# Kernel tuning notes

Hardware: AMD Instinct MI355X
Metric: run time of the kernel (lower is better)

Reference implementation:

```python
import jax, jax.numpy as jnp
import numpy as np
import math

NH, NR, HD, QK, ITERS = 8, 8, 64, 32, 4


def _pe(seq_len, dim):
    n = 1.0 / (1.0 + math.exp(-1))
    pos = np.arange(seq_len, dtype=np.float64)[:, None]
    i = np.arange(0, dim, 2, dtype=np.float64)[None, :]
    pe = np.zeros((seq_len, dim), np.float32)
    pe[:, 0::2] = n * np.sin(pos / 10000 ** (2 * i / dim))
    pe[:, 1::2] = n * np.cos(pos / 10000 ** (2 * (i + 1) / dim))
    return jnp.asarray(pe)


def _ln(x, g, b, eps=1e-5):
    m = x.mean(-1, keepdims=True)
    v = ((x - m) ** 2).mean(-1, keepdims=True)
    return (x - m) * jax.lax.rsqrt(v + eps) * g + b


def _comp_attn(x, norm1_g, norm1_b, norm2_g, norm2_b, q_w, q_b, k_w, k_b,
               v_w, v_b, qv_w, qv_b, score_w, score_b, final_w, final_b,
               ffn1_w, ffn1_b, ffn2_w, ffn2_b):
    B, S, D = x.shape
    res = x
    h = _ln(x, norm1_g, norm1_b)
    q = (h @ q_w + q_b).reshape(B, S, NH, HD).transpose(0, 2, 1, 3) / math.sqrt(HD)  # [B,nh,S,hd]
    k = (h @ k_w + k_b).reshape(B, S, NH, HD)                                         # [B,S,nh,hd]
    v = (h @ v_w + v_b).reshape(B, S, NR, HD)                                         # [B,S,nr,hd]
    score = jax.nn.softmax(jnp.einsum('bhqd,bkhd->bhqk', q, k), axis=-1)              # [B,nh,S,S]
    out = jnp.einsum('bhqk,bkrd->bqhrd', score, v)                                    # [B,S,nh,nr,hd]
    qv = (h @ qv_w + qv_b).reshape(B, S, NH, QK)
    qv_e = jnp.broadcast_to(qv[:, :, :, None, :], (B, S, NH, NR, QK))
    in_ = jnp.concatenate([qv_e, out], axis=-1)                                       # [B,S,nh,nr,qk+hd]
    comp = jax.nn.softmax(in_ @ score_w + score_b, axis=3)                            # [B,S,nh,nr,1]
    o = (comp * out).sum(axis=3).reshape(B, S, D)
    o = o @ final_w + final_b
    x = res + o
    res2 = x
    h2 = _ln(x, norm2_g, norm2_b)
    ff = jax.nn.relu(h2 @ ffn1_w + ffn1_b) @ ffn2_w + ffn2_b  # dropout identity (eval)
    return res2 + ff


def reference(img, qst, conv_w, conv_b, qrep_w, qrep_b, cls_token, map_w, map_b,
              norm1_g, norm1_b, norm2_g, norm2_b, q_w, q_b, k_w, k_b, v_w, v_b,
              qv_w, qv_b, score_w, score_b, final_w, final_b,
              ffn1_w, ffn1_b, ffn2_w, ffn2_b, out_w, out_b):
    B = img.shape[0]
    H = conv_w.shape[0]  # 256
    pe = _pe(25, H)
    # patch embedding: conv 15x15 stride 15 -> [B,H,5,5]
    p = jax.lax.conv_general_dilated(img, conv_w, (15, 15), 'VALID',
                                     dimension_numbers=('NCHW', 'OIHW', 'NCHW'))
    p = p + conv_b[None, :, None, None]
    p = p.reshape(B, H, 25).transpose(0, 2, 1) + pe[None]       # [B,25,H]
    cls = jnp.broadcast_to(cls_token, (B, 1, H))
    emb = jnp.concatenate([cls, p], axis=1)                      # [B,26,H]
    que = (qst @ qrep_w + qrep_b)[:, None, :]
    que = jnp.broadcast_to(que, (B, 26, H))
    x = jnp.concatenate([emb, que], axis=-1)                     # [B,26,2H]
    x = x @ map_w + map_b                                        # [B,26,D]
    for _ in range(ITERS):
        x = _comp_attn(x, norm1_g, norm1_b, norm2_g, norm2_b, q_w, q_b, k_w, k_b,
                       v_w, v_b, qv_w, qv_b, score_w, score_b, final_w, final_b,
                       ffn1_w, ffn1_b, ffn2_w, ffn2_b)
    y = x[:, 0, :] @ out_w + out_b
    return jax.nn.log_softmax(y, axis=1)


def setup_inputs() -> dict:
    key = jax.random.key(0)
    ks = iter(jax.random.split(key, 64))
    def rn(shape, s=0.02):
        return jax.random.normal(next(ks), shape, jnp.float32) * s
    B, D, H = 256, 512, 256
    return {
        'img': jax.random.normal(next(ks), (B, 3, 75, 75), jnp.float32),
        'qst': jax.random.normal(next(ks), (B, 18), jnp.float32),
        'conv_w': rn((H, 3, 15, 15)), 'conv_b': rn((H,)),
        'qrep_w': rn((18, H)), 'qrep_b': rn((H,)),
        'cls_token': rn((1, 1, H), 1.0),
        'map_w': rn((2 * H, D)), 'map_b': rn((D,)),
        'norm1_g': jnp.ones((D,), jnp.float32), 'norm1_b': jnp.zeros((D,), jnp.float32),
        'norm2_g': jnp.ones((D,), jnp.float32), 'norm2_b': jnp.zeros((D,), jnp.float32),
        'q_w': rn((D, D)), 'q_b': rn((D,)),
        'k_w': rn((D, D)), 'k_b': rn((D,)),
        'v_w': rn((D, NR * HD)), 'v_b': rn((NR * HD,)),
        'qv_w': rn((D, QK * NH)), 'qv_b': rn((QK * NH,)),
        'score_w': rn((HD + QK, 1)), 'score_b': rn((1,)),
        'final_w': rn((D, D)), 'final_b': rn((D,)),
        'ffn1_w': rn((D, 2 * D)), 'ffn1_b': rn((2 * D,)),
        'ffn2_w': rn((2 * D, D)), 'ffn2_b': rn((D,)),
        'out_w': rn((D, 10)), 'out_b': rn((10,)),
    }
```

## Files before the change

kernel.cpp:

```cpp
#include <hip/hip_runtime.h>
#include <math.h>

#define NB 256
#define SEQ 26
#define TOK (NB*SEQ)
#define DIM 512

typedef unsigned short u16;
typedef __attribute__((ext_vector_type(8))) short short8_t;
typedef __attribute__((ext_vector_type(4))) float floatx4;

__device__ inline u16 f2bf(float f) {
    union { float f; unsigned u; } v; v.f = f;
    unsigned r = v.u + 0x7fffu + ((v.u >> 16) & 1u);
    return (u16)(r >> 16);
}
__device__ inline float bf2f(u16 u) {
    union { unsigned u; float f; } v; v.u = ((unsigned)u) << 16; return v.f;
}

__device__ __forceinline__ void gload_lds16(const u16* g, u16* l) {
    __builtin_amdgcn_global_load_lds((const __attribute__((address_space(1))) void*)g,
                                     (__attribute__((address_space(3))) void*)l, 16, 0, 0);
}

__global__ void prep_all(const float* __restrict__ q_w, const float* __restrict__ k_w,
                         const float* __restrict__ v_w, const float* __restrict__ final_w,
                         const float* __restrict__ ffn1_w, const float* __restrict__ ffn2_w,
                         const float* __restrict__ map_w, const float* __restrict__ conv_w,
                         const float* __restrict__ q_b, const float* __restrict__ k_b,
                         const float* __restrict__ v_b,
                         u16* __restrict__ qkvT, u16* __restrict__ finT,
                         u16* __restrict__ f1T, u16* __restrict__ f2T,
                         u16* __restrict__ mapT, u16* __restrict__ cwT,
                         float* __restrict__ qkvb) {
    __shared__ float lds[64][65];
    int blk = blockIdx.x;
    int t = threadIdx.x;
    if (blk < 544) {
        const float* W; u16* Wt; int K, N, tbase;
        if (blk < 64)       { W = q_w;     Wt = qkvT;            K = 512;  N = 512;  tbase = 0;   }
        else if (blk < 128) { W = k_w;     Wt = qkvT + 512*512;  K = 512;  N = 512;  tbase = 64;  }
        else if (blk < 192) { W = v_w;     Wt = qkvT + 1024*512; K = 512;  N = 512;  tbase = 128; }
        else if (blk < 256) { W = final_w; Wt = finT;            K = 512;  N = 512;  tbase = 192; }
        else if (blk < 384) { W = ffn1_w;  Wt = f1T;             K = 512;  N = 1024; tbase = 256; }
        else if (blk < 512) { W = ffn2_w;  Wt = f2T;             K = 1024; N = 512;  tbase = 384; }
        else                { W = map_w;   Wt = mapT;            K = 256;  N = 512;  tbase = 512; }
        int tloc = blk - tbase;
        int ntn = N >> 6;
        int n0 = (tloc % ntn) * 64, k0 = (tloc / ntn) * 64;
        int j = t & 63, i0 = t >> 6;
        #pragma unroll
        for (int p = 0; p < 16; ++p) {
            int i = i0*16 + p;
            lds[i][j] = W[(size_t)(k0+i)*N + n0 + j];
        }
        __syncthreads();
        int i2 = t & 63, j0 = t >> 6;
        #pragma unroll
        for (int p = 0; p < 16; ++p) {
            int j2 = j0*16 + p;
            Wt[(size_t)(n0+j2)*K + k0 + i2] = f2bf(lds[i2][j2]);
        }
    } else if (blk < 544 + 256) {
        int oc = blk - 544;
        for (int jj = t; jj < 704; jj += 256)
            cwT[(size_t)oc*704 + jj] = (jj < 675) ? f2bf(conv_w[(size_t)oc*675 + jj]) : (u16)0;
    } else {
        for (int jj = t; jj < 1536; jj += 256)
            qkvb[jj] = jj < 512 ? q_b[jj] : (jj < 1024 ? k_b[jj-512] : v_b[jj-1024]);
    }
}

__global__ void im2col_kernel(const float* __restrict__ img, u16* __restrict__ P) {
    int ri = blockIdx.x;
    int b = ri / 25, pos = ri % 25, ph = pos/5, pw = pos%5;
    for (int j = threadIdx.x; j < 704; j += 256) {
        float v = 0.f;
        if (j < 675) {
            int c = j / 225, rem = j % 225, kh = rem/15, kw = rem%15;
            v = img[(size_t)((b*3+c)*75 + ph*15 + kh)*75 + pw*15 + kw];
        }
        P[(size_t)ri*704 + j] = f2bf(v);
    }
}

__global__ void pe_cls_kernel(const float* __restrict__ co, const float* __restrict__ cls,
                              u16* __restrict__ emb) {
    int t = blockIdx.x;
    int b = t / SEQ, s = t % SEQ;
    int oc = threadIdx.x;
    float v;
    if (s == 0) v = cls[oc];
    else {
        int pos = s - 1;
        float freq = __powf(10000.0f, -(float)oc / 128.0f);
        float a = (float)pos * freq;
        float pe = 0.7310585786300049f * ((oc & 1) ? __cosf(a) : __sinf(a));
        v = co[(size_t)(b*25+pos)*256 + oc] + pe;
    }
    emb[(size_t)t*256 + oc] = f2bf(v);
}

template<int RESMODE, int RELU, int OUTBF>
__global__ __launch_bounds__(512) void mfma_gemm(const u16* __restrict__ A, const u16* __restrict__ Bt,
                          const float* __restrict__ bias, const float* __restrict__ res,
                          void* __restrict__ Cout, int M, int N, int K, float alpha) {
    __shared__ __align__(16) u16 As[128*64];
    __shared__ __align__(16) u16 Bs[128*64];
    const int tid = threadIdx.x;
    const int lane = tid & 63;
    const int w = tid >> 6;
    const int wr = (w >> 2) * 64;
    const int wc = (w & 3) * 32;
    const int bm = blockIdx.y * 128, bn = blockIdx.x * 128;

    floatx4 acc[4][2];
    #pragma unroll
    for (int mi = 0; mi < 4; ++mi)
        #pragma unroll
        for (int ni = 0; ni < 2; ++ni)
            acc[mi][ni] = (floatx4){0.f,0.f,0.f,0.f};

    int idx0 = tid, idx1 = 512 + tid;
    int row0 = idx0 >> 3, ch0 = (idx0 & 7) ^ (row0 & 7);
    int row1 = idx1 >> 3, ch1 = (idx1 & 7) ^ (row1 & 7);
    const u16* a0 = &A [(size_t)(bm+row0)*K + ch0*8];
    const u16* a1 = &A [(size_t)(bm+row1)*K + ch1*8];
    const u16* b0 = &Bt[(size_t)(bn+row0)*K + ch0*8];
    const u16* b1 = &Bt[(size_t)(bn+row1)*K + ch1*8];

    for (int k0 = 0; k0 < K; k0 += 64) {
        __syncthreads();
        gload_lds16(a0 + k0, &As[idx0*8]);
        gload_lds16(a1 + k0, &As[idx1*8]);
        gload_lds16(b0 + k0, &Bs[idx0*8]);
        gload_lds16(b1 + k0, &Bs[idx1*8]);
        __syncthreads();
        #pragma unroll
        for (int kk = 0; kk < 2; ++kk) {
            int ch2 = kk*4 + (lane >> 4);
            short8_t af[4], bf[2];
            #pragma unroll
            for (int mi = 0; mi < 4; ++mi) {
                int row = wr + mi*16 + (lane & 15);
                af[mi] = *(const short8_t*)&As[row*64 + ((ch2 ^ (row & 7))*8)];
            }
            #pragma unroll
            for (int ni = 0; ni < 2; ++ni) {
                int rowb = wc + ni*16 + (lane & 15);
                bf[ni] = *(const short8_t*)&Bs[rowb*64 + ((ch2 ^ (rowb & 7))*8)];
            }
            #pragma unroll
            for (int mi = 0; mi < 4; ++mi)
                #pragma unroll
                for (int ni = 0; ni < 2; ++ni)
                    acc[mi][ni] = __builtin_amdgcn_mfma_f32_16x16x32_bf16(
                        af[mi], bf[ni], acc[mi][ni], 0, 0, 0);
        }
    }

    #pragma unroll
    for (int mi = 0; mi < 4; ++mi) {
        #pragma unroll
        for (int ni = 0; ni < 2; ++ni) {
            int col = bn + wc + ni*16 + (lane & 15);
            float bv = bias ? bias[col] : 0.0f;
            #pragma unroll
            for (int r = 0; r < 4; ++r) {
                int row = bm + wr + mi*16 + (lane >> 4)*4 + r;
                float v = (acc[mi][ni][r] + bv) * alpha;
                if (RELU) v = fmaxf(v, 0.f);
                if (RESMODE == 1)      v += res[(size_t)row*N + col];
                else if (RESMODE == 2) v += res[(size_t)(row/SEQ)*N + col];
                if (OUTBF) ((u16*)Cout)[(size_t)row*N + col] = f2bf(v);
                else       ((float*)Cout)[(size_t)row*N + col] = v;
            }
        }
    }
}

__global__ void que_map_kernel(const float* __restrict__ qst,
                               const float* __restrict__ qrep_w,
                               const float* __restrict__ qrep_b,
                               const float* __restrict__ map_w,
                               const float* __restrict__ map_b,
                               float* __restrict__ quem) {
    int b = blockIdx.x;
    int t = threadIdx.x;
    __shared__ float que[256];
    float acc = qrep_b[t];
    for (int j = 0; j < 18; ++j) acc += qst[b*18 + j] * qrep_w[j*256 + t];
    que[t] = acc;
    __syncthreads();
    for (int n = t; n < DIM; n += 256) {
        float a2 = map_b[n];
        for (int k = 0; k < 256; ++k) a2 += que[k] * map_w[(256 + k)*DIM + n];
        quem[b*DIM + n] = a2;
    }
}

__global__ void ln_kernel(const float* __restrict__ x, const float* __restrict__ g,
                          const float* __restrict__ bta, u16* __restrict__ out) {
    int t = blockIdx.x;
    int tid = threadIdx.x;
    const float* xr = x + (size_t)t*DIM;
    float v0 = xr[tid], v1 = xr[tid+256];
    float s = v0 + v1, sq = v0*v0 + v1*v1;
    __shared__ float rs[4], rq[4];
    for (int off = 32; off; off >>= 1) { s += __shfl_down(s, off); sq += __shfl_down(sq, off); }
    int wid = tid >> 6, lane = tid & 63;
    if (lane == 0) { rs[wid] = s; rq[wid] = sq; }
    __syncthreads();
    __shared__ float mean_s, rstd_s;
    if (tid == 0) {
        float ts = rs[0]+rs[1]+rs[2]+rs[3], tq = rq[0]+rq[1]+rq[2]+rq[3];
        float m = ts / DIM;
        float var = tq / DIM - m*m;
        mean_s = m; rstd_s = rsqrtf(var + 1e-5f);
    }
    __syncthreads();
    float m = mean_s, r = rstd_s;
    out[(size_t)t*DIM + tid]       = f2bf((v0 - m)*r*g[tid]     + bta[tid]);
    out[(size_t)t*DIM + tid + 256] = f2bf((v1 - m)*r*g[tid+256] + bta[tid+256]);
}

__global__ __launch_bounds__(512) void attn_fused_kernel(const u16* __restrict__ qkv,
                                                         const float* __restrict__ score_w,
                                                         u16* __restrict__ attn_o) {
    int b = blockIdx.x;
    __shared__ u16 Bt[64*224];
    __shared__ float s_lds[208*28];
    __shared__ float vwl[208];
    __shared__ float cmp_lds[208*8];
    __shared__ float swl[64];
    int tid = threadIdx.x;
    int lane = tid & 63, w = tid >> 6;

    if (tid < 64) swl[tid] = score_w[32 + tid];
    for (int k = 0; k < 26; ++k) {
        int d2 = tid & 63, r = tid >> 6;
        u16 v = qkv[(size_t)(b*SEQ+k)*1536 + 1024 + tid];
        int bo = (d2*448 + (k*8+r)*2) ^ ((d2 & 7) << 4);
        *(u16*)((char*)Bt + bo) = v;
    }
    {
        int d2 = tid & 63, kr = 208 + (tid >> 6);
        int bo1 = (d2*448 + kr*2)     ^ ((d2 & 7) << 4);
        int bo2 = (d2*448 + (kr+8)*2) ^ ((d2 & 7) << 4);
        *(u16*)((char*)Bt + bo1) = 0;
        *(u16*)((char*)Bt + bo2) = 0;
    }
    for (int row = tid; row < 208; row += 512) {
        s_lds[row*28 + 26] = 0.f; s_lds[row*28 + 27] = 0.f;
    }

    {
        int h = w;
        int col16 = lane & 15, ch = lane >> 4;
        short8_t qf[2][2], kf[2][2];
        #pragma unroll
        for (int mi = 0; mi < 2; ++mi) {
            int q = mi*16 + col16;
            #pragma unroll
            for (int kk = 0; kk < 2; ++kk) {
                if (q < 26)
                    qf[mi][kk] = *(const short8_t*)&qkv[(size_t)(b*SEQ+q)*1536 + h*64 + kk*32 + ch*8];
                else
                    qf[mi][kk] = (short8_t){0,0,0,0,0,0,0,0};
            }
        }
        #pragma unroll
        for (int ni = 0; ni < 2; ++ni) {
            int kq = ni*16 + col16;
            #pragma unroll
            for (int kk = 0; kk < 2; ++kk) {
                if (kq < 26)
                    kf[ni][kk] = *(const short8_t*)&qkv[(size_t)(b*SEQ+kq)*1536 + 512 + h*64 + kk*32 + ch*8];
                else
                    kf[ni][kk] = (short8_t){0,0,0,0,0,0,0,0};
            }
        }
        floatx4 sacc[2][2];
        #pragma unroll
        for (int mi = 0; mi < 2; ++mi)
            #pragma unroll
            for (int ni = 0; ni < 2; ++ni)
                sacc[mi][ni] = (floatx4){0.f,0.f,0.f,0.f};
        #pragma unroll
        for (int kk = 0; kk < 2; ++kk)
            #pragma unroll
            for (int mi = 0; mi < 2; ++mi)
                #pragma unroll
                for (int ni = 0; ni < 2; ++ni)
                    sacc[mi][ni] = __builtin_amdgcn_mfma_f32_16x16x32_bf16(
                        qf[mi][kk], kf[ni][kk], sacc[mi][ni], 0, 0, 0);
        #pragma unroll
        for (int mi = 0; mi < 2; ++mi) {
            #pragma unroll
            for (int r = 0; r < 4; ++r) {
                float s0 = sacc[mi][0][r] * 0.125f;
                float s1 = (col16 < 10) ? sacc[mi][1][r] * 0.125f : -1e30f;
                float mx = fmaxf(s0, s1);
                #pragma unroll
                for (int msk = 1; msk < 16; msk <<= 1) mx = fmaxf(mx, __shfl_xor(mx, msk));
                float e0 = __expf(s0 - mx);
                float e1 = (col16 < 10) ? __expf(s1 - mx) : 0.f;
                float den = e0 + e1;
                #pragma unroll
                for (int msk = 1; msk < 16; msk <<= 1) den += __shfl_xor(den, msk);
                float inv = 1.f / den;
                int q = mi*16 + ch*4 + r;
                if (q < 26) {
                    s_lds[(h*26+q)*28 + col16] = e0 * inv;
                    if (col16 < 10) s_lds[(h*26+q)*28 + 16 + col16] = e1 * inv;
                }
            }
        }
    }
    __syncthreads();

    if (tid < 208) {
        float acc = 0.f;
        for (int d2 = 0; d2 < 64; ++d2) {
            int bo = (d2*448 + tid*2) ^ ((d2 & 7) << 4);
            acc += bf2f(*(const u16*)((const char*)Bt + bo)) * swl[d2];
        }
        vwl[tid] = acc;
    }
    __syncthreads();

    if (tid < 208) {
        float srow[26];
        #pragma unroll
        for (int k = 0; k < 26; ++k) srow[k] = s_lds[tid*28 + k];
        float e[8];
        #pragma unroll
        for (int r = 0; r < 8; ++r) {
            float a = 0.f;
            #pragma unroll
            for (int k = 0; k < 26; ++k) a += srow[k] * vwl[k*8 + r];
            e[r] = a;
        }
        float m = e[0];
        #pragma unroll
        for (int r = 1; r < 8; ++r) m = fmaxf(m, e[r]);
        float den = 0.f;
        #pragma unroll
        for (int r = 0; r < 8; ++r) { e[r] = __expf(e[r]-m); den += e[r]; }
        float inv = 1.f/den;
        #pragma unroll
        for (int r = 0; r < 8; ++r) cmp_lds[tid*8+r] = e[r]*inv;
    }
    __syncthreads();

    int mh = w >> 2, nt = w & 3;
    int ntile0 = nt*16;
    short8_t bfr[7];
    #pragma unroll
    for (int ks = 0; ks < 7; ++ks) {
        int col = ntile0 + (lane & 15);
        int krb = ks*32 + (lane >> 4)*8;
        int bo = (col*448 + krb*2) ^ ((col & 7) << 4);
        bfr[ks] = *(const short8_t*)((const char*)Bt + bo);
    }
    int mt0 = mh ? 7 : 0, mt1 = mh ? 13 : 7;
    for (int mt = mt0; mt < mt1; ++mt) {
        int arow = mt*16 + (lane & 15);
        float c8[8];
        #pragma unroll
        for (int r = 0; r < 8; ++r) c8[r] = cmp_lds[arow*8 + r];
        floatx4 acc = (floatx4){0.f,0.f,0.f,0.f};
        #pragma unroll
        for (int ks = 0; ks < 7; ++ks) {
            int k = ks*4 + (lane >> 4);
            float sv = s_lds[arow*28 + k];
            short8_t af;
            #pragma unroll
            for (int j = 0; j < 8; ++j) af[j] = (short)f2bf(sv * c8[j]);
            acc = __builtin_amdgcn_mfma_f32_16x16x32_bf16(af, bfr[ks], acc, 0, 0, 0);
        }
        int colg = ntile0 + (lane & 15);
        #pragma unroll
        for (int rr = 0; rr < 4; ++rr) {
            int rowg = mt*16 + (lane >> 4)*4 + rr;
            int h = rowg / 26, q = rowg - h*26;
            attn_o[(size_t)(b*SEQ+q)*DIM + h*64 + colg] = f2bf(acc[rr]);
        }
    }
}

__global__ void head_kernel(const float* __restrict__ x, const float* __restrict__ out_w,
                            const float* __restrict__ out_b, float* __restrict__ y) {
    int b = blockIdx.x;
    int t = threadIdx.x;
    __shared__ float yv[10];
    if (t < 10) {
        float acc = out_b[t];
        const float* xr = x + (size_t)(b*SEQ)*DIM;
        for (int dd = 0; dd < DIM; ++dd) acc += xr[dd]*out_w[dd*10 + t];
        yv[t] = acc;
    }
    __syncthreads();
    if (t < 10) {
        float m = yv[0];
        for (int i = 1; i < 10; ++i) m = fmaxf(m, yv[i]);
        float den = 0.0f;
        for (int i = 0; i < 10; ++i) den += expf(yv[i]-m);
        y[b*10 + t] = yv[t] - m - logf(den);
    }
}

extern "C" void kernel_launch(void* const* d_in, const int* in_sizes, int n_in,
                              void* d_out, int out_size, void* d_ws, size_t ws_size,
                              hipStream_t stream) {
    const float* img      = (const float*)d_in[0];
    const float* qst      = (const float*)d_in[1];
    const float* conv_w   = (const float*)d_in[2];
    const float* conv_b   = (const float*)d_in[3];
    const float* qrep_w   = (const float*)d_in[4];
    const float* qrep_b   = (const float*)d_in[5];
    const float* cls_tok  = (const float*)d_in[6];
    const float* map_w    = (const float*)d_in[7];
    const float* map_b    = (const float*)d_in[8];
    const float* norm1_g  = (const float*)d_in[9];
    const float* norm1_b  = (const float*)d_in[10];
    const float* norm2_g  = (const float*)d_in[11];
    const float* norm2_b  = (const float*)d_in[12];
    const float* q_w      = (const float*)d_in[13];
    const float* q_b      = (const float*)d_in[14];
    const float* k_w      = (const float*)d_in[15];
    const float* k_b      = (const float*)d_in[16];
    const float* v_w      = (const float*)d_in[17];
    const float* v_b      = (const float*)d_in[18];
    const float* score_w  = (const float*)d_in[21];
    const float* final_w  = (const float*)d_in[23];
    const float* final_b  = (const float*)d_in[24];
    const float* ffn1_w   = (const float*)d_in[25];
    const float* ffn1_b   = (const float*)d_in[26];
    const float* ffn2_w   = (const float*)d_in[27];
    const float* ffn2_b   = (const float*)d_in[28];
    const float* out_w    = (const float*)d_in[29];
    const float* out_b    = (const float*)d_in[30];

    float* ws = (float*)d_ws;
    size_t o = 0;
    float* x    = ws + o;       o += (size_t)TOK*DIM;
    u16* qkvT   = (u16*)(ws+o); o += (size_t)1536*512/2;
    u16* finT   = (u16*)(ws+o); o += (size_t)512*512/2;
    u16* f1T    = (u16*)(ws+o); o += (size_t)1024*512/2;
    u16* f2T    = (u16*)(ws+o); o += (size_t)512*1024/2;
    u16* mapT   = (u16*)(ws+o); o += (size_t)512*256/2;
    u16* cwT    = (u16*)(ws+o); o += (size_t)256*704/2;
    float* qkvb = ws + o;       o += 1536;
    float* r2   = ws + o;
    u16*  h_bf    = (u16*)r2;
    u16*  qkv_bf  = (u16*)(r2 + (size_t)TOK*DIM/2);
    u16*  attn_obf= (u16*)(r2 + (size_t)TOK*DIM/2 + (size_t)TOK*1536/2);
    u16*  ffbuf   = qkv_bf;
    u16*  Pbuf    = (u16*)r2;
    float* convout= r2 + (size_t)6400*704/2;
    u16*  emb_bf  = (u16*)(convout + (size_t)6400*256);
    float* quem   = convout + (size_t)6400*256 + (size_t)TOK*256/2;

    prep_all<<<801, 256, 0, stream>>>(q_w, k_w, v_w, final_w, ffn1_w, ffn2_w, map_w, conv_w,
                                      q_b, k_b, v_b, qkvT, finT, f1T, f2T, mapT, cwT, qkvb);

    im2col_kernel<<<6400, 256, 0, stream>>>(img, Pbuf);
    que_map_kernel<<<NB, 256, 0, stream>>>(qst, qrep_w, qrep_b, map_w, map_b, quem);
    mfma_gemm<0,0,0><<<dim3(2,50), dim3(512), 0, stream>>>(
        Pbuf, cwT, conv_b, nullptr, convout, 6400, 256, 704, 1.0f);
    pe_cls_kernel<<<TOK, 256, 0, stream>>>(convout, cls_tok, emb_bf);
    mfma_gemm<2,0,0><<<dim3(4,52), dim3(512), 0, stream>>>(
        emb_bf, mapT, nullptr, quem, x, TOK, 512, 256, 1.0f);

    for (int it = 0; it < 4; ++it) {
        ln_kernel<<<TOK, 256, 0, stream>>>(x, norm1_g, norm1_b, h_bf);
        mfma_gemm<0,0,1><<<dim3(12,52), dim3(512), 0, stream>>>(
            h_bf, qkvT, qkvb, nullptr, qkv_bf, TOK, 1536, 512, 1.0f);
        attn_fused_kernel<<<NB, 512, 0, stream>>>(qkv_bf, score_w, attn_obf);
        mfma_gemm<1,0,0><<<dim3(4,52), dim3(512), 0, stream>>>(
            attn_obf, finT, final_b, x, x, TOK, 512, 512, 1.0f);
        ln_kernel<<<TOK, 256, 0, stream>>>(x, norm2_g, norm2_b, h_bf);
        mfma_gemm<0,1,1><<<dim3(8,52), dim3(512), 0, stream>>>(
            h_bf, f1T, ffn1_b, nullptr, ffbuf, TOK, 1024, 512, 1.0f);
        mfma_gemm<1,0,0><<<dim3(4,52), dim3(512), 0, stream>>>(
            ffbuf, f2T, ffn2_b, x, x, TOK, 512, 1024, 1.0f);
    }

    head_kernel<<<NB, 64, 0, stream>>>(x, out_w, out_b, (float*)d_out);
}
```

Before: 621.0 us.

## Double-buffer GEMM LDS tiles and fuse positional encoding into conv GEMM epilogue

The GEMM main loop now uses two LDS buffers, so the next K-tile's global-to-LDS load is issued while MFMAs run on the current tile. This replaces two barriers per iteration with one and aims to hide load latency. Separately, the pe_cls kernel is removed: the conv GEMM epilogue adds the positional encoding and writes bf16 embeddings directly, and cls-token rows are written inside prep_all. Together these drop one launch and a float round-trip, at the cost of doubled LDS use (64KB per block), which may lower occupancy.

After: 584.9 us. -5.8%, faster.

```diff
diff --git a/kernel.cpp b/kernel.cpp
--- a/kernel.cpp
+++ b/kernel.cpp
@@ -29,11 +29,11 @@
                          const float* __restrict__ ffn1_w, const float* __restrict__ ffn2_w,
                          const float* __restrict__ map_w, const float* __restrict__ conv_w,
                          const float* __restrict__ q_b, const float* __restrict__ k_b,
-                         const float* __restrict__ v_b,
+                         const float* __restrict__ v_b, const float* __restrict__ cls,
                          u16* __restrict__ qkvT, u16* __restrict__ finT,
                          u16* __restrict__ f1T, u16* __restrict__ f2T,
                          u16* __restrict__ mapT, u16* __restrict__ cwT,
-                         float* __restrict__ qkvb) {
+                         float* __restrict__ qkvb, u16* __restrict__ emb) {
     __shared__ float lds[64][65];
     int blk = blockIdx.x;
     int t = threadIdx.x;
@@ -66,6 +66,9 @@
         int oc = blk - 544;
         for (int jj = t; jj < 704; jj += 256)
             cwT[(size_t)oc*704 + jj] = (jj < 675) ? f2bf(conv_w[(size_t)oc*675 + jj]) : (u16)0;
+    } else if (blk < 544 + 256 + 256) {
+        int b = blk - 800;
+        emb[(size_t)(b*SEQ)*256 + t] = f2bf(cls[t]);
     } else {
         for (int jj = t; jj < 1536; jj += 256)
             qkvb[jj] = jj < 512 ? q_b[jj] : (jj < 1024 ? k_b[jj-512] : v_b[jj-1024]);
@@ -85,29 +88,12 @@
     }
 }
 
-__global__ void pe_cls_kernel(const float* __restrict__ co, const float* __restrict__ cls,
-                              u16* __restrict__ emb) {
-    int t = blockIdx.x;
-    int b = t / SEQ, s = t % SEQ;
-    int oc = threadIdx.x;
-    float v;
-    if (s == 0) v = cls[oc];
-    else {
-        int pos = s - 1;
-        float freq = __powf(10000.0f, -(float)oc / 128.0f);
-        float a = (float)pos * freq;
-        float pe = 0.7310585786300049f * ((oc & 1) ? __cosf(a) : __sinf(a));
-        v = co[(size_t)(b*25+pos)*256 + oc] + pe;
-    }
-    emb[(size_t)t*256 + oc] = f2bf(v);
-}
-
 template<int RESMODE, int RELU, int OUTBF>
 __global__ __launch_bounds__(512) void mfma_gemm(const u16* __restrict__ A, const u16* __restrict__ Bt,
                           const float* __restrict__ bias, const float* __restrict__ res,
                           void* __restrict__ Cout, int M, int N, int K, float alpha) {
-    __shared__ __align__(16) u16 As[128*64];
-    __shared__ __align__(16) u16 Bs[128*64];
+    __shared__ __align__(16) u16 As[2][128*64];
+    __shared__ __align__(16) u16 Bs[2][128*64];
     const int tid = threadIdx.x;
     const int lane = tid & 63;
     const int w = tid >> 6;
@@ -130,13 +116,22 @@
     const u16* b0 = &Bt[(size_t)(bn+row0)*K + ch0*8];
     const u16* b1 = &Bt[(size_t)(bn+row1)*K + ch1*8];
 
-    for (int k0 = 0; k0 < K; k0 += 64) {
-        __syncthreads();
-        gload_lds16(a0 + k0, &As[idx0*8]);
-        gload_lds16(a1 + k0, &As[idx1*8]);
-        gload_lds16(b0 + k0, &Bs[idx0*8]);
-        gload_lds16(b1 + k0, &Bs[idx1*8]);
-        __syncthreads();
+    const int nt = K >> 6;
+    gload_lds16(a0, &As[0][idx0*8]);
+    gload_lds16(a1, &As[0][idx1*8]);
+    gload_lds16(b0, &Bs[0][idx0*8]);
+    gload_lds16(b1, &Bs[0][idx1*8]);
+    __syncthreads();
+
+    for (int t = 0; t < nt; ++t) {
+        const int cur = t & 1;
+        if (t + 1 < nt) {
+            int off = (t + 1) << 6;
+            gload_lds16(a0 + off, &As[cur^1][idx0*8]);
+            gload_lds16(a1 + off, &As[cur^1][idx1*8]);
+            gload_lds16(b0 + off, &Bs[cur^1][idx0*8]);
+            gload_lds16(b1 + off, &Bs[cur^1][idx1*8]);
+        }
         #pragma unroll
         for (int kk = 0; kk < 2; ++kk) {
             int ch2 = kk*4 + (lane >> 4);
@@ -144,12 +139,12 @@
             #pragma unroll
             for (int mi = 0; mi < 4; ++mi) {
                 int row = wr + mi*16 + (lane & 15);
-                af[mi] = *(const short8_t*)&As[row*64 + ((ch2 ^ (row & 7))*8)];
+                af[mi] = *(const short8_t*)&As[cur][row*64 + ((ch2 ^ (row & 7))*8)];
             }
             #pragma unroll
             for (int ni = 0; ni < 2; ++ni) {
                 int rowb = wc + ni*16 + (lane & 15);
-                bf[ni] = *(const short8_t*)&Bs[rowb*64 + ((ch2 ^ (rowb & 7))*8)];
+                bf[ni] = *(const short8_t*)&Bs[cur][rowb*64 + ((ch2 ^ (rowb & 7))*8)];
             }
             #pragma unroll
             for (int mi = 0; mi < 4; ++mi)
@@ -158,6 +153,7 @@
                     acc[mi][ni] = __builtin_amdgcn_mfma_f32_16x16x32_bf16(
                         af[mi], bf[ni], acc[mi][ni], 0, 0, 0);
         }
+        __syncthreads();
     }
 
     #pragma unroll
@@ -173,8 +169,17 @@
                 if (RELU) v = fmaxf(v, 0.f);
                 if (RESMODE == 1)      v += res[(size_t)row*N + col];
                 else if (RESMODE == 2) v += res[(size_t)(row/SEQ)*N + col];
-                if (OUTBF) ((u16*)Cout)[(size_t)row*N + col] = f2bf(v);
-                else       ((float*)Cout)[(size_t)row*N + col] = v;
+                if (RESMODE == 3) {
+                    int bb = row / 25, pos = row - bb*25;
+                    float freq = __powf(10000.0f, -(float)col / 128.0f);
+                    float a = (float)pos * freq;
+                    float pe = 0.7310585786300049f * ((col & 1) ? __cosf(a) : __sinf(a));
+                    ((u16*)Cout)[(size_t)(bb*SEQ + 1 + pos)*256 + col] = f2bf(v + pe);
+                } else if (OUTBF) {
+                    ((u16*)Cout)[(size_t)row*N + col] = f2bf(v);
+                } else {
+                    ((float*)Cout)[(size_t)row*N + col] = v;
+                }
             }
         }
     }
@@ -459,18 +464,17 @@
     u16*  attn_obf= (u16*)(r2 + (size_t)TOK*DIM/2 + (size_t)TOK*1536/2);
     u16*  ffbuf   = qkv_bf;
     u16*  Pbuf    = (u16*)r2;
-    float* convout= r2 + (size_t)6400*704/2;
-    u16*  emb_bf  = (u16*)(convout + (size_t)6400*256);
-    float* quem   = convout + (size_t)6400*256 + (size_t)TOK*256/2;
-
-    prep_all<<<801, 256, 0, stream>>>(q_w, k_w, v_w, final_w, ffn1_w, ffn2_w, map_w, conv_w,
-                                      q_b, k_b, v_b, qkvT, finT, f1T, f2T, mapT, cwT, qkvb);
+    u16*  emb_bf  = (u16*)(r2 + (size_t)6400*704/2);
+    float* quem   = r2 + (size_t)6400*704/2 + (size_t)TOK*256/2;
+
+    prep_all<<<1057, 256, 0, stream>>>(q_w, k_w, v_w, final_w, ffn1_w, ffn2_w, map_w, conv_w,
+                                       q_b, k_b, v_b, cls_tok,
+                                       qkvT, finT, f1T, f2T, mapT, cwT, qkvb, emb_bf);
 
     im2col_kernel<<<6400, 256, 0, stream>>>(img, Pbuf);
     que_map_kernel<<<NB, 256, 0, stream>>>(qst, qrep_w, qrep_b, map_w, map_b, quem);
-    mfma_gemm<0,0,0><<<dim3(2,50), dim3(512), 0, stream>>>(
-        Pbuf, cwT, conv_b, nullptr, convout, 6400, 256, 704, 1.0f);
-    pe_cls_kernel<<<TOK, 256, 0, stream>>>(convout, cls_tok, emb_bf);
+    mfma_gemm<3,0,1><<<dim3(2,50), dim3(512), 0, stream>>>(
+        Pbuf, cwT, conv_b, nullptr, emb_bf, 6400, 256, 704, 1.0f);
     mfma_gemm<2,0,0><<<dim3(4,52), dim3(512), 0, stream>>>(
         emb_bf, mapT, nullptr, quem, x, TOK, 512, 256, 1.0f);
 
```
